# Performance work log

Measured on AMD Instinct MI355X. Metric: run time of the kernel, lower is better.

## Reference

```python
import jax, jax.numpy as jnp
import numpy as np

N_GENES = 20000
UNITS = 10000
DEG = 32
BATCH = 128

def setup_inputs() -> dict:
    key = jax.random.key(0)
    k1, k2, k3, k4 = jax.random.split(key, 4)
    feature = jax.random.normal(k1, (BATCH, N_GENES), dtype=jnp.float32)
    ppi = jax.random.randint(k2, (UNITS, DEG), 0, N_GENES, dtype=jnp.int64)
    kernel = jax.random.normal(k3, (UNITS,), dtype=jnp.float32)
    bias = jax.random.normal(k4, (UNITS,), dtype=jnp.float32)
    return {"feature": feature, "ppi": ppi, "kernel": kernel, "bias": bias}

def reference(feature, ppi, kernel, bias):
    # gather along gene axis: [B, UNITS, DEG]
    h = jnp.abs(feature[:, ppi])
    # sum over neighbors -> [B, UNITS]
    h = jnp.sum(h, axis=-1)
    h = h * kernel + bias
    return jnp.tanh(h)
```

## Files before the change

kernel.cpp:

```cpp
#include <hip/hip_runtime.h>
#include <math.h>

#define N_GENES 20000
#define UNITS   10000
#define DEG     32
#define BATCH   128

__global__ __launch_bounds__(256) void transpose_abs_kernel(
    const float* __restrict__ in, float* __restrict__ out)
{
    __shared__ float tile[32][33];
    const int g0 = blockIdx.x * 32;
    const int b0 = blockIdx.y * 32;
    const int tx = threadIdx.x;
    const int ty = threadIdx.y;
#pragma unroll
    for (int i = 0; i < 32; i += 8) {
        tile[ty + i][tx] = fabsf(in[(size_t)(b0 + ty + i) * N_GENES + (g0 + tx)]);
    }
    __syncthreads();
#pragma unroll
    for (int i = 0; i < 32; i += 8) {
        out[(size_t)(g0 + ty + i) * BATCH + (b0 + tx)] = tile[tx][ty + i];
    }
}

__global__ __launch_bounds__(256) void gather_unit_kernel(
    const float* __restrict__ featT,
    const int*   __restrict__ ppi,
    const float* __restrict__ kernelw,
    const float* __restrict__ bias,
    float*       __restrict__ out)
{
    __shared__ int idx[16 * DEG];
    const int tid = threadIdx.x;
    const int u0  = blockIdx.x * 16;

    {
        const int* src = ppi + (size_t)u0 * DEG;
        idx[tid]       = src[tid];
        idx[tid + 256] = src[tid + 256];
    }
    __syncthreads();

    const int b     = tid & 127;
    const int ubase = (tid >> 7) * 8;

    float acc[8] = {0.f, 0.f, 0.f, 0.f, 0.f, 0.f, 0.f, 0.f};

#pragma unroll 4
    for (int d = 0; d < DEG; ++d) {
#pragma unroll
        for (int j = 0; j < 8; ++j) {
            const int g = idx[(ubase + j) * DEG + d];
            acc[j] += featT[(size_t)g * BATCH + b];
        }
    }

    float res[8];
#pragma unroll
    for (int j = 0; j < 8; ++j) {
        const int u = u0 + ubase + j;
        const float h = acc[j] * kernelw[u] + bias[u];
        const float e = __expf(2.f * h);
        res[j] = 1.f - 2.f / (e + 1.f);
    }

    float4* o = (float4*)(out + (size_t)b * UNITS + u0 + ubase);
    o[0] = make_float4(res[0], res[1], res[2], res[3]);
    o[1] = make_float4(res[4], res[5], res[6], res[7]);
}

extern "C" void kernel_launch(void* const* d_in, const int* in_sizes, int n_in,
                              void* d_out, int out_size, void* d_ws, size_t ws_size,
                              hipStream_t stream) {
    const float* feature = (const float*)d_in[0];
    const int*   ppi     = (const int*)d_in[1];
    const float* kernelw = (const float*)d_in[2];
    const float* bias    = (const float*)d_in[3];
    float* out   = (float*)d_out;
    float* featT = (float*)d_ws;

    dim3 g1(N_GENES / 32, BATCH / 32);
    dim3 b1(32, 8);
    transpose_abs_kernel<<<g1, b1, 0, stream>>>(feature, featT);

    gather_unit_kernel<<<UNITS / 16, 256, 0, stream>>>(featT, ppi, kernelw, bias, out);
}
```

Before: 88.07 us.

## Store transposed abs features in fp16 and gather half2 per lane

The transpose kernel now writes |feature| as fp16, halving the intermediate buffer and the bytes moved by the random gather. The gather kernel is remapped so each wave handles two units, with each lane loading a half2 covering two batch entries and accumulating in fp32. Blocks now cover 8 units instead of 16. This trades input precision (fp16 rounding before summation) and narrower, more scattered output stores for reduced gather bandwidth.

```diff
diff --git a/kernel.cpp b/kernel.cpp
--- a/kernel.cpp
+++ b/kernel.cpp
@@ -1,4 +1,5 @@
 #include <hip/hip_runtime.h>
+#include <hip/hip_fp16.h>
 #include <math.h>
 
 #define N_GENES 20000
@@ -6,8 +7,8 @@
 #define DEG     32
 #define BATCH   128
 
-__global__ __launch_bounds__(256) void transpose_abs_kernel(
-    const float* __restrict__ in, float* __restrict__ out)
+__global__ __launch_bounds__(256) void transpose_abs_f16_kernel(
+    const float* __restrict__ in, __half* __restrict__ out)
 {
     __shared__ float tile[32][33];
     const int g0 = blockIdx.x * 32;
@@ -15,60 +16,60 @@
     const int tx = threadIdx.x;
     const int ty = threadIdx.y;
 #pragma unroll
-    for (int i = 0; i < 32; i += 8) {
+    for (int i = 0; i < 32; i += 8)
         tile[ty + i][tx] = fabsf(in[(size_t)(b0 + ty + i) * N_GENES + (g0 + tx)]);
-    }
     __syncthreads();
 #pragma unroll
-    for (int i = 0; i < 32; i += 8) {
-        out[(size_t)(g0 + ty + i) * BATCH + (b0 + tx)] = tile[tx][ty + i];
-    }
+    for (int i = 0; i < 32; i += 8)
+        out[(size_t)(g0 + ty + i) * BATCH + (b0 + tx)] = __float2half(tile[tx][ty + i]);
 }
 
 __global__ __launch_bounds__(256) void gather_unit_kernel(
-    const float* __restrict__ featT,
+    const __half2* __restrict__ featT,
     const int*   __restrict__ ppi,
     const float* __restrict__ kernelw,
     const float* __restrict__ bias,
     float*       __restrict__ out)
 {
-    __shared__ int idx[16 * DEG];
+    __shared__ int idx[8 * DEG];
     const int tid = threadIdx.x;
-    const int u0  = blockIdx.x * 16;
+    const int u0  = blockIdx.x * 8;
 
-    {
-        const int* src = ppi + (size_t)u0 * DEG;
-        idx[tid]       = src[tid];
-        idx[tid + 256] = src[tid + 256];
-    }
+    idx[tid] = ppi[(size_t)u0 * DEG + tid];
     __syncthreads();
 
-    const int b     = tid & 127;
-    const int ubase = (tid >> 7) * 8;
+    const int lane = tid & 63;
+    const int w    = tid >> 6;
+    const int ub   = w * 2;
 
-    float acc[8] = {0.f, 0.f, 0.f, 0.f, 0.f, 0.f, 0.f, 0.f};
+    float2 acc0 = {0.f, 0.f}, acc1 = {0.f, 0.f};
 
-#pragma unroll 4
+#pragma unroll 8
     for (int d = 0; d < DEG; ++d) {
-#pragma unroll
-        for (int j = 0; j < 8; ++j) {
-            const int g = idx[(ubase + j) * DEG + d];
-            acc[j] += featT[(size_t)g * BATCH + b];
-        }
+        const int g0 = idx[ub * DEG + d];
+        const int g1 = idx[(ub + 1) * DEG + d];
+        const float2 f0 = __half22float2(featT[(size_t)g0 * 64 + lane]);
+        const float2 f1 = __half22float2(featT[(size_t)g1 * 64 + lane]);
+        acc0.x += f0.x; acc0.y += f0.y;
+        acc1.x += f1.x; acc1.y += f1.y;
     }
 
-    float res[8];
-#pragma unroll
-    for (int j = 0; j < 8; ++j) {
-        const int u = u0 + ubase + j;
-        const float h = acc[j] * kernelw[u] + bias[u];
-        const float e = __expf(2.f * h);
-        res[j] = 1.f - 2.f / (e + 1.f);
-    }
+    const int u  = u0 + ub;
+    const float k0 = kernelw[u],     k1 = kernelw[u + 1];
+    const float c0 = bias[u],        c1 = bias[u + 1];
 
-    float4* o = (float4*)(out + (size_t)b * UNITS + u0 + ubase);
-    o[0] = make_float4(res[0], res[1], res[2], res[3]);
-    o[1] = make_float4(res[4], res[5], res[6], res[7]);
+    const float h00 = acc0.x * k0 + c0;
+    const float h01 = acc1.x * k1 + c1;
+    const float h10 = acc0.y * k0 + c0;
+    const float h11 = acc1.y * k1 + c1;
+    const float r00 = 1.f - 2.f / (__expf(2.f * h00) + 1.f);
+    const float r01 = 1.f - 2.f / (__expf(2.f * h01) + 1.f);
+    const float r10 = 1.f - 2.f / (__expf(2.f * h10) + 1.f);
+    const float r11 = 1.f - 2.f / (__expf(2.f * h11) + 1.f);
+
+    const int b = lane * 2;
+    *(float2*)(out + (size_t)b       * UNITS + u) = make_float2(r00, r01);
+    *(float2*)(out + (size_t)(b + 1) * UNITS + u) = make_float2(r10, r11);
 }
 
 extern "C" void kernel_launch(void* const* d_in, const int* in_sizes, int n_in,
@@ -79,11 +80,12 @@
     const float* kernelw = (const float*)d_in[2];
     const float* bias    = (const float*)d_in[3];
     float* out   = (float*)d_out;
-    float* featT = (float*)d_ws;
+    __half* featT = (__half*)d_ws;
 
     dim3 g1(N_GENES / 32, BATCH / 32);
     dim3 b1(32, 8);
-    transpose_abs_kernel<<<g1, b1, 0, stream>>>(feature, featT);
+    transpose_abs_f16_kernel<<<g1, b1, 0, stream>>>(feature, featT);
 
-    gather_unit_kernel<<<UNITS / 16, 256, 0, stream>>>(featT, ppi, kernelw, bias, out);
+    gather_unit_kernel<<<UNITS / 8, 256, 0, stream>>>(
+        (const __half2*)featT, ppi, kernelw, bias, out);
 }
```

Result: faster. 79.96 us (-9.2%).

## Store transposed abs features as fp16 and gather with 16-byte vector loads

Applied to the files above, without the earlier changes.

The transposed |feature| table is now written in half precision, which halves the workspace write traffic and the bytes fetched by the gather. The gather kernel is reorganised so each 16-lane quarter-wavefront loads 8 halves per lane with one float4 load and covers a different neighbour. Partial sums are combined across quarters with cross-lane shuffles, staged in shared memory, and written out with coalesced float4 stores. The cost is fp16 rounding of the inputs before summation, which can loosen numerical agreement with the fp32 reference.

```diff
diff --git a/kernel.cpp b/kernel.cpp
--- a/kernel.cpp
+++ b/kernel.cpp
@@ -1,13 +1,15 @@
 #include <hip/hip_runtime.h>
+#include <hip/hip_fp16.h>
 #include <math.h>
 
 #define N_GENES 20000
 #define UNITS   10000
 #define DEG     32
 #define BATCH   128
+#define UPB     16
 
-__global__ __launch_bounds__(256) void transpose_abs_kernel(
-    const float* __restrict__ in, float* __restrict__ out)
+__global__ __launch_bounds__(256) void transpose_abs_f16_kernel(
+    const float* __restrict__ in, __half* __restrict__ out)
 {
     __shared__ float tile[32][33];
     const int g0 = blockIdx.x * 32;
@@ -15,26 +17,26 @@
     const int tx = threadIdx.x;
     const int ty = threadIdx.y;
 #pragma unroll
-    for (int i = 0; i < 32; i += 8) {
+    for (int i = 0; i < 32; i += 8)
         tile[ty + i][tx] = fabsf(in[(size_t)(b0 + ty + i) * N_GENES + (g0 + tx)]);
-    }
     __syncthreads();
 #pragma unroll
-    for (int i = 0; i < 32; i += 8) {
-        out[(size_t)(g0 + ty + i) * BATCH + (b0 + tx)] = tile[tx][ty + i];
-    }
+    for (int i = 0; i < 32; i += 8)
+        out[(size_t)(g0 + ty + i) * BATCH + (b0 + tx)] = __float2half(tile[tx][ty + i]);
 }
 
 __global__ __launch_bounds__(256) void gather_unit_kernel(
-    const float* __restrict__ featT,
+    const __half* __restrict__ featT,
     const int*   __restrict__ ppi,
     const float* __restrict__ kernelw,
     const float* __restrict__ bias,
     float*       __restrict__ out)
 {
-    __shared__ int idx[16 * DEG];
+    __shared__ int   idx[UPB * DEG];
+    __shared__ float res[UPB][BATCH];
+
     const int tid = threadIdx.x;
-    const int u0  = blockIdx.x * 16;
+    const int u0  = blockIdx.x * UPB;
 
     {
         const int* src = ppi + (size_t)u0 * DEG;
@@ -43,32 +45,55 @@
     }
     __syncthreads();
 
-    const int b     = tid & 127;
-    const int ubase = (tid >> 7) * 8;
+    const int lane = tid & 63;
+    const int w    = tid >> 6;
+    const int q    = lane >> 4;
+    const int c    = lane & 15;
 
-    float acc[8] = {0.f, 0.f, 0.f, 0.f, 0.f, 0.f, 0.f, 0.f};
-
-#pragma unroll 4
-    for (int d = 0; d < DEG; ++d) {
+#pragma unroll 2
+    for (int uu = 0; uu < 4; ++uu) {
+        const int ul = w * 4 + uu;
+        float acc[8] = {0.f,0.f,0.f,0.f,0.f,0.f,0.f,0.f};
+#pragma unroll
+        for (int it = 0; it < 8; ++it) {
+            const int g = idx[ul * DEG + it * 4 + q];
+            const float4 raw = *(const float4*)(featT + (size_t)g * BATCH + c * 8);
+            const __half2* h2 = (const __half2*)&raw;
+#pragma unroll
+            for (int p = 0; p < 4; ++p) {
+                const float2 f = __half22float2(h2[p]);
+                acc[2 * p]     += f.x;
+                acc[2 * p + 1] += f.y;
+            }
+        }
+        const int u   = u0 + ul;
+        const float kk = kernelw[u];
+        const float bb = bias[u];
 #pragma unroll
         for (int j = 0; j < 8; ++j) {
-            const int g = idx[(ubase + j) * DEG + d];
-            acc[j] += featT[(size_t)g * BATCH + b];
+            float v = acc[j];
+            v += __shfl_xor(v, 16, 64);
+            v += __shfl_xor(v, 32, 64);
+            acc[j] = v;
+        }
+        if (q == 0) {
+#pragma unroll
+            for (int j = 0; j < 8; ++j) {
+                const float h = acc[j] * kk + bb;
+                res[ul][c * 8 + j] = 1.f - 2.f / (__expf(2.f * h) + 1.f);
+            }
         }
     }
+    __syncthreads();
 
-    float res[8];
+    const int b    = tid >> 1;
+    const int half = tid & 1;
+    float v[8];
 #pragma unroll
-    for (int j = 0; j < 8; ++j) {
-        const int u = u0 + ubase + j;
-        const float h = acc[j] * kernelw[u] + bias[u];
-        const float e = __expf(2.f * h);
-        res[j] = 1.f - 2.f / (e + 1.f);
-    }
-
-    float4* o = (float4*)(out + (size_t)b * UNITS + u0 + ubase);
-    o[0] = make_float4(res[0], res[1], res[2], res[3]);
-    o[1] = make_float4(res[4], res[5], res[6], res[7]);
+    for (int j = 0; j < 8; ++j) v[j] = res[half * 8 + j][b];
+    float4* o = (float4*)(out + (size_t)b * UNITS + u0 + half * 8);
+    o[0] = make_float4(v[0], v[1], v[2], v[3]);
+    o[1] = make_float4(v[4], v[5], v[6], v[7]);
 }
 
 extern "C" void kernel_launch(void* const* d_in, const int* in_sizes, int n_in,
@@ -79,11 +104,12 @@
     const float* kernelw = (const float*)d_in[2];
     const float* bias    = (const float*)d_in[3];
     float* out   = (float*)d_out;
-    float* featT = (float*)d_ws;
+    __half* featT = (__half*)d_ws;
 
     dim3 g1(N_GENES / 32, BATCH / 32);
     dim3 b1(32, 8);
-    transpose_abs_kernel<<<g1, b1, 0, stream>>>(feature, featT);
+    transpose_abs_f16_kernel<<<g1, b1, 0, stream>>>(feature, featT);
 
-    gather_unit_kernel<<<UNITS / 16, 256, 0, stream>>>(featT, ppi, kernelw, bias, out);
+    gather_unit_kernel<<<UNITS / UPB, 256, 0, stream>>>(
+        featT, ppi, kernelw, bias, out);
 }
```

New measurement: 80.60 us. 8.5% less time.
